# Kernel tuning notes

Measured on AMD Instinct MI355X. Metric: run time of the kernel, lower is better.

Reference implementation:

```python
import jax, jax.numpy as jnp
import numpy as np

B, T, E, H, HD, FF = 2, 2048, 1024, 16, 64, 4096
LN_EPS = 1e-5


def _ln(x, g, b):
    mu = jnp.mean(x, axis=-1, keepdims=True)
    var = jnp.var(x, axis=-1, keepdims=True)
    return (x - mu) * jax.lax.rsqrt(var + LN_EPS) * g + b


def setup_inputs() -> dict:
    key = jax.random.key(0)
    ks = jax.random.split(key, 8)
    s = 0.02
    return {
        "x": jax.random.normal(ks[0], (B, T, E), jnp.float32),
        "Wq": jax.random.normal(ks[1], (H, E, HD), jnp.float32) * s,
        "Wk": jax.random.normal(ks[2], (H, E, HD), jnp.float32) * s,
        "Wv": jax.random.normal(ks[3], (H, E, HD), jnp.float32) * s,
        "Wproj": jax.random.normal(ks[4], (E, E), jnp.float32) * s,
        "bproj": jnp.zeros((E,), jnp.float32),
        "W1": jax.random.normal(ks[5], (E, FF), jnp.float32) * s,
        "b1": jnp.zeros((FF,), jnp.float32),
        "W2": jax.random.normal(ks[6], (FF, E), jnp.float32) * s,
        "b2": jnp.zeros((E,), jnp.float32),
        "g1": jnp.ones((E,), jnp.float32),
        "be1": jnp.zeros((E,), jnp.float32),
        "g2": jnp.ones((E,), jnp.float32),
        "be2": jnp.zeros((E,), jnp.float32),
    }


def reference(x, Wq, Wk, Wv, Wproj, bproj, W1, b1, W2, b2, g1, be1, g2, be2):
    # --- pre-LN multi-head causal self-attention (dropout = eval/identity) ---
    h = _ln(x, g1, be1)  # [B,T,E]
    q = jnp.einsum('btd,hde->bhte', h, Wq)  # [B,H,T,HD]
    k = jnp.einsum('btd,hde->bhte', h, Wk)
    v = jnp.einsum('btd,hde->bhte', h, Wv)
    # NOTE: original code scales by C**-0.5 where C = embedding_dim (not head_size)
    scale = E ** (-0.5)
    wei = jnp.einsum('bhqe,bhke->bhqk', q, k) * scale  # [B,H,T,T]
    causal = jnp.tril(jnp.ones((T, T), dtype=bool))
    wei = jnp.where(causal, wei, -jnp.inf)
    attn = jax.nn.softmax(wei, axis=-1)
    o = jnp.einsum('bhqk,bhke->bhqe', attn, v)  # [B,H,T,HD]
    o = o.transpose(0, 2, 1, 3).reshape(B, T, E)  # concat heads
    o = o @ Wproj + bproj
    x = x + o
    # --- ReLU FFN ---
    h2 = _ln(x, g2, be2)
    f = jax.nn.relu(h2 @ W1 + b1) @ W2 + b2
    return x + f
```

## Files before the change

kernel.cpp:

```cpp
#include <hip/hip_runtime.h>
#include <hip/hip_bf16.h>
#include <stdint.h>

#define T_SEQ 2048
#define E_DIM 1024
#define H_NUM 16
#define HD_DIM 64
#define FF_DIM 4096
#define B_NUM 2
#define N_TOK (B_NUM * T_SEQ)

typedef unsigned short ushort_t;
typedef __bf16 bf16x8 __attribute__((ext_vector_type(8)));
typedef float f32x4 __attribute__((ext_vector_type(4)));

__device__ __forceinline__ float bf2f(ushort_t u) {
    return __uint_as_float(((unsigned)u) << 16);
}
__device__ __forceinline__ ushort_t f2bf(float f) {
    unsigned u = __float_as_uint(f);
    u += 0x7fffu + ((u >> 16) & 1u);
    return (ushort_t)(u >> 16);
}
__device__ __forceinline__ float bflo(unsigned u) { return __uint_as_float(u << 16); }
__device__ __forceinline__ float bfhi(unsigned u) { return __uint_as_float(u & 0xffff0000u); }

__device__ __forceinline__ void async_copy16(const ushort_t* g, ushort_t* l) {
    __builtin_amdgcn_global_load_lds(
        (__attribute__((address_space(1))) uint32_t*)(ushort_t*)g,
        (__attribute__((address_space(3))) uint32_t*)l, 16, 0, 0);
}

__global__ __launch_bounds__(256) void ln_kernel(const float* __restrict__ x,
                                                 const float* __restrict__ g,
                                                 const float* __restrict__ be,
                                                 ushort_t* __restrict__ out) {
    __shared__ float red[8];
    const int row = blockIdx.x, tid = threadIdx.x;
    const float* xr = x + (size_t)row * E_DIM;
    float4 v = ((const float4*)xr)[tid];
    float s = v.x + v.y + v.z + v.w;
    float sq = v.x * v.x + v.y * v.y + v.z * v.z + v.w * v.w;
    for (int off = 32; off; off >>= 1) {
        s += __shfl_xor(s, off);
        sq += __shfl_xor(sq, off);
    }
    const int wid = tid >> 6, lane = tid & 63;
    if (lane == 0) { red[wid] = s; red[4 + wid] = sq; }
    __syncthreads();
    s = red[0] + red[1] + red[2] + red[3];
    sq = red[4] + red[5] + red[6] + red[7];
    const float mean = s * (1.0f / E_DIM);
    const float var = sq * (1.0f / E_DIM) - mean * mean;
    const float rstd = rsqrtf(var + 1e-5f);
    float4 gv = ((const float4*)g)[tid];
    float4 bv = ((const float4*)be)[tid];
    unsigned o0 = f2bf((v.x - mean) * rstd * gv.x + bv.x);
    unsigned o1 = f2bf((v.y - mean) * rstd * gv.y + bv.y);
    unsigned o2 = f2bf((v.z - mean) * rstd * gv.z + bv.z);
    unsigned o3 = f2bf((v.w - mean) * rstd * gv.w + bv.w);
    uint2 w;
    w.x = o0 | (o1 << 16);
    w.y = o2 | (o3 << 16);
    ((uint2*)(out + (size_t)row * E_DIM))[tid] = w;
}

__global__ __launch_bounds__(256) void reduce_ln_kernel(const ushort_t* __restrict__ p0,
                                                        const ushort_t* __restrict__ p1,
                                                        const float* __restrict__ x,
                                                        const float* __restrict__ bias,
                                                        const float* __restrict__ g,
                                                        const float* __restrict__ be,
                                                        float* __restrict__ x1,
                                                        ushort_t* __restrict__ h2) {
    __shared__ float red[8];
    const int row = blockIdx.x, tid = threadIdx.x;
    uint2 u0 = ((const uint2*)(p0 + (size_t)row * E_DIM))[tid];
    uint2 u1 = ((const uint2*)(p1 + (size_t)row * E_DIM))[tid];
    float4 xv = ((const float4*)(x + (size_t)row * E_DIM))[tid];
    float4 bv = ((const float4*)bias)[tid];
    float4 v;
    v.x = xv.x + bv.x + bflo(u0.x) + bflo(u1.x);
    v.y = xv.y + bv.y + bfhi(u0.x) + bfhi(u1.x);
    v.z = xv.z + bv.z + bflo(u0.y) + bflo(u1.y);
    v.w = xv.w + bv.w + bfhi(u0.y) + bfhi(u1.y);
    ((float4*)(x1 + (size_t)row * E_DIM))[tid] = v;
    float s = v.x + v.y + v.z + v.w;
    float sq = v.x * v.x + v.y * v.y + v.z * v.z + v.w * v.w;
    for (int off = 32; off; off >>= 1) {
        s += __shfl_xor(s, off);
        sq += __shfl_xor(sq, off);
    }
    const int wid = tid >> 6, lane = tid & 63;
    if (lane == 0) { red[wid] = s; red[4 + wid] = sq; }
    __syncthreads();
    s = red[0] + red[1] + red[2] + red[3];
    sq = red[4] + red[5] + red[6] + red[7];
    const float mean = s * (1.0f / E_DIM);
    const float var = sq * (1.0f / E_DIM) - mean * mean;
    const float rstd = rsqrtf(var + 1e-5f);
    float4 gv = ((const float4*)g)[tid];
    float4 ev = ((const float4*)be)[tid];
    unsigned o0 = f2bf((v.x - mean) * rstd * gv.x + ev.x);
    unsigned o1 = f2bf((v.y - mean) * rstd * gv.y + ev.y);
    unsigned o2 = f2bf((v.z - mean) * rstd * gv.z + ev.z);
    unsigned o3 = f2bf((v.w - mean) * rstd * gv.w + ev.w);
    uint2 w;
    w.x = o0 | (o1 << 16);
    w.y = o2 | (o3 << 16);
    ((uint2*)(h2 + (size_t)row * E_DIM))[tid] = w;
}

__global__ __launch_bounds__(256) void reduce_out_kernel(const ushort_t* __restrict__ p0,
                                                         const ushort_t* __restrict__ p1,
                                                         const float* __restrict__ x1,
                                                         const float* __restrict__ bias,
                                                         float* __restrict__ out) {
    const int row = blockIdx.x, tid = threadIdx.x;
    uint2 u0 = ((const uint2*)(p0 + (size_t)row * E_DIM))[tid];
    uint2 u1 = ((const uint2*)(p1 + (size_t)row * E_DIM))[tid];
    float4 xv = ((const float4*)(x1 + (size_t)row * E_DIM))[tid];
    float4 bv = ((const float4*)bias)[tid];
    float4 v;
    v.x = xv.x + bv.x + bflo(u0.x) + bflo(u1.x);
    v.y = xv.y + bv.y + bfhi(u0.x) + bfhi(u1.x);
    v.z = xv.z + bv.z + bflo(u0.y) + bflo(u1.y);
    v.w = xv.w + bv.w + bfhi(u0.y) + bfhi(u1.y);
    ((float4*)(out + (size_t)row * E_DIM))[tid] = v;
}

__global__ __launch_bounds__(256) void transpose_kernel(const float* __restrict__ in,
                                                        ushort_t* __restrict__ out,
                                                        int R, int C) {
    __shared__ ushort_t tile[32][33];
    const int c0 = blockIdx.x * 32, r0 = blockIdx.y * 32;
    const int tx = threadIdx.x, ty = threadIdx.y;
#pragma unroll
    for (int i = 0; i < 32; i += 8) tile[ty + i][tx] = f2bf(in[(size_t)(r0 + ty + i) * C + (c0 + tx)]);
    __syncthreads();
#pragma unroll
    for (int i = 0; i < 32; i += 8) out[(size_t)(c0 + ty + i) * R + (r0 + tx)] = tile[tx][ty + i];
}

__global__ __launch_bounds__(256) void transpose_qkv_kernel(const float* __restrict__ Wq,
                                                            const float* __restrict__ Wk,
                                                            const float* __restrict__ Wv,
                                                            ushort_t* __restrict__ outT) {
    __shared__ ushort_t tile[32][33];
    const int z = blockIdx.z, m = z >> 4, hh = z & 15;
    const float* in = ((m == 0) ? Wq : ((m == 1) ? Wk : Wv)) + (size_t)hh * E_DIM * HD_DIM;
    ushort_t* out = outT + (size_t)(m * E_DIM + hh * HD_DIM) * E_DIM;
    const int c0 = blockIdx.x * 32, r0 = blockIdx.y * 32;
    const int tx = threadIdx.x, ty = threadIdx.y;
#pragma unroll
    for (int i = 0; i < 32; i += 8) tile[ty + i][tx] = f2bf(in[(size_t)(r0 + ty + i) * HD_DIM + (c0 + tx)]);
    __syncthreads();
#pragma unroll
    for (int i = 0; i < 32; i += 8) out[(size_t)(c0 + ty + i) * E_DIM + (r0 + tx)] = tile[tx][ty + i];
}

template <int MODE, int BK>
__global__ __launch_bounds__(256) void gemm_bt(const ushort_t* __restrict__ A,
                                               const ushort_t* __restrict__ BT,
                                               const float* __restrict__ bias,
                                               const float* __restrict__ resid,
                                               void* __restrict__ C0,
                                               ushort_t* __restrict__ C1,
                                               ushort_t* __restrict__ C2,
                                               int M, int N, int K, int lda) {
    __shared__ __align__(16) ushort_t lds_a[2][128 * BK];
    __shared__ __align__(16) ushort_t lds_b[2][128 * BK];
    const int tid = threadIdx.x;
    const int id = blockIdx.y * gridDim.x + blockIdx.x;
    const int band = id & 7, within = id >> 3;
    const int rpb = gridDim.y >> 3;
    const int by = band * rpb + (within % rpb);
    const int bx = within / rpb;
    const int m0 = by * 128, n0 = bx * 128;
    const int koff = blockIdx.z * K;
    const int wave = tid >> 6, lane = tid & 63;
    const int wm = (wave >> 1) * 64, wn = (wave & 1) * 64;
    const int quad = lane >> 4, l16 = lane & 15;
    f32x4 acc[4][4] = {};

    const int nk = K / BK;
    auto stage = [&](int kt, int buf) {
        const int k0 = koff + kt * BK;
#pragma unroll
        for (int it = 0; it < BK / 16; ++it) {
            const int ci = it * 256 + tid;
            const int kk = ci >> 9;
            const int rem = ci & 511;
            const int r = rem >> 2, kc = rem & 3;
            const int gk = k0 + kk * 32 + kc * 8;
            async_copy16(A + (size_t)(m0 + r) * lda + gk, &lds_a[buf][ci * 8]);
            async_copy16(BT + (size_t)(n0 + r) * lda + gk, &lds_b[buf][ci * 8]);
        }
    };
    stage(0, 0);

#pragma unroll 1
    for (int kt = 0; kt < nk; ++kt) {
        __syncthreads();
        if (kt + 1 < nk) stage(kt + 1, (kt + 1) & 1);
        const ushort_t* la = lds_a[kt & 1];
        const ushort_t* lb = lds_b[kt & 1];
#pragma unroll
        for (int kk = 0; kk < BK / 32; ++kk) {
            const ushort_t* lak = la + kk * 4096;
            const ushort_t* lbk = lb + kk * 4096;
            bf16x8 af[4], bfr[4];
#pragma unroll
            for (int i = 0; i < 4; i++) af[i] = *(const bf16x8*)&lak[(wm + i * 16 + l16) * 32 + quad * 8];
#pragma unroll
            for (int i = 0; i < 4; i++) bfr[i] = *(const bf16x8*)&lbk[(wn + i * 16 + l16) * 32 + quad * 8];
#pragma unroll
            for (int im = 0; im < 4; im++)
#pragma unroll
                for (int in = 0; in < 4; in++)
                    acc[im][in] = __builtin_amdgcn_mfma_f32_16x16x32_bf16(af[im], bfr[in], acc[im][in], 0, 0, 0);
        }
    }

    ushort_t* pc = nullptr;
    if (MODE == 3) pc = (blockIdx.z == 0) ? (ushort_t*)C0 : C1;
#pragma unroll
    for (int im = 0; im < 4; im++) {
#pragma unroll
        for (int in = 0; in < 4; in++) {
            const int col = n0 + wn + in * 16 + l16;
            float bv = (MODE == 1 || MODE == 2) ? bias[col] : 0.0f;
#pragma unroll
            for (int r = 0; r < 4; r++) {
                const int row = m0 + wm + im * 16 + quad * 4 + r;
                float v = acc[im][in][r] + bv;
                if (MODE == 2) v = fmaxf(v, 0.0f);
                if (MODE == 1) v += resid[(size_t)row * N + col];
                if (MODE == 0) {
                    const int mat = col >> 10, c = col & 1023, hh = c >> 6, d = c & 63;
                    const int bb = row >> 11, tt = row & 2047;
                    const int bh = bb * H_NUM + hh;
                    size_t idx;
                    ushort_t* dst;
                    if (mat == 0) {
                        idx = ((((size_t)bh * 32 + (tt >> 6)) * 8 + (d >> 3)) * 64 + (tt & 63)) * 8 + (d & 7);
                        dst = (ushort_t*)C0;
                        v *= 0.0450842048f;
                    } else if (mat == 1) {
                        idx = ((((size_t)bh * 32 + (tt >> 6)) * 8 + (d >> 3)) * 64 + (tt & 63)) * 8 + (d & 7);
                        dst = C1;
                    } else {
                        idx = ((((size_t)bh * 32 + (tt >> 6)) * 8 + ((tt & 63) >> 3)) * 64 + d) * 8 + (tt & 7);
                        dst = C2;
                    }
                    dst[idx] = f2bf(v);
                } else if (MODE == 1) {
                    ((float*)C0)[(size_t)row * N + col] = v;
                } else if (MODE == 2) {
                    ((ushort_t*)C0)[(size_t)row * N + col] = f2bf(v);
                } else {
                    pc[(size_t)row * N + col] = f2bf(v);
                }
            }
        }
    }
    (void)M;
}

__global__ __launch_bounds__(256, 2) void attn_flash(const ushort_t* __restrict__ qP,
                                                     const ushort_t* __restrict__ kP,
                                                     const ushort_t* __restrict__ vP,
                                                     ushort_t* __restrict__ o) {
    __shared__ __align__(16) ushort_t P_lds[4][32 * 72];
    __shared__ __align__(16) float Ored[2][32][68];
    __shared__ float Lred[2][32];
    const int h = blockIdx.x, p = blockIdx.y, b = blockIdx.z;
    const int bh = b * H_NUM + h;
    const int tid = threadIdx.x;
    const int wave = tid >> 6, lane = tid & 63;
    const int wr = wave >> 1, ws = wave & 1;
    const int quad = lane >> 4, l16 = lane & 15;
    ushort_t* Pw = P_lds[wave];
    const ushort_t* kbase = kP + (size_t)bh * 32 * 4096;
    const ushort_t* vbase = vP + (size_t)bh * 32 * 4096;
    bf16x8 onesf;
#pragma unroll
    for (int j = 0; j < 8; ++j) onesf[j] = (__bf16)1.0f;

#pragma unroll 1
    for (int phase = 0; phase < 2; ++phase) {
        const int qt = (phase == 0) ? (31 - p) : p;
        const int nkt = qt + 1;
        const ushort_t* qbase = qP + ((size_t)bh * 32 + qt) * 4096;
        bf16x8 qf[2][2];
#pragma unroll
        for (int rg = 0; rg < 2; ++rg)
#pragma unroll
            for (int kk = 0; kk < 2; ++kk)
                qf[rg][kk] = *(const bf16x8*)&qbase[((kk * 4 + quad) * 64 + wr * 32 + rg * 16 + l16) * 8];
        f32x4 oacc[2][4] = {};
        f32x4 lacc[2] = {};
        __syncthreads();
        bf16x8 kf[8], vf[8];
        {
            const ushort_t* kb = kbase + (size_t)ws * 4096;
#pragma unroll
            for (int i = 0; i < 8; ++i)
                kf[i] = *(const bf16x8*)&kb[(((i >> 2) * 4 + quad) * 64 + (i & 3) * 16 + l16) * 8];
        }
#pragma unroll 1
        for (int kt = ws; kt < nkt; kt += 2) {
            f32x4 sacc[2][4] = {};
            __builtin_amdgcn_s_setprio(1);
#pragma unroll
            for (int kk = 0; kk < 2; ++kk)
#pragma unroll
                for (int kg = 0; kg < 4; ++kg)
#pragma unroll
                    for (int rg = 0; rg < 2; ++rg)
                        sacc[rg][kg] = __builtin_amdgcn_mfma_f32_16x16x32_bf16(
                            qf[rg][kk], kf[kk * 4 + kg], sacc[rg][kg], 0, 0, 0);
            __builtin_amdgcn_s_setprio(0);
            {
                const ushort_t* vb = vbase + (size_t)kt * 4096;
#pragma unroll
                for (int i = 0; i < 8; ++i)
                    vf[i] = *(const bf16x8*)&vb[(((i >> 2) * 4 + quad) * 64 + (i & 3) * 16 + l16) * 8];
            }
            if (kt + 2 < nkt) {
                const ushort_t* kb = kbase + (size_t)(kt + 2) * 4096;
#pragma unroll
                for (int i = 0; i < 8; ++i)
                    kf[i] = *(const bf16x8*)&kb[(((i >> 2) * 4 + quad) * 64 + (i & 3) * 16 + l16) * 8];
            }
#pragma unroll
            for (int rg = 0; rg < 2; ++rg)
#pragma unroll
                for (int kg = 0; kg < 4; ++kg) {
                    f32x4 sv = sacc[rg][kg];
                    if (kt == qt) {
                        const int jc = kg * 16 + l16;
#pragma unroll
                        for (int r = 0; r < 4; ++r)
                            if (jc > wr * 32 + rg * 16 + quad * 4 + r) sv[r] = -3.0e38f;
                    }
#pragma unroll
                    for (int r = 0; r < 4; ++r) {
                        const float e = exp2f(sv[r]);
                        Pw[(rg * 16 + quad * 4 + r) * 72 + kg * 16 + l16] =
                            (ushort_t)(__float_as_uint(e) >> 16);
                    }
                }
            __builtin_amdgcn_s_setprio(1);
#pragma unroll
            for (int kk = 0; kk < 2; ++kk)
#pragma unroll
                for (int rg = 0; rg < 2; ++rg) {
                    bf16x8 pf = *(const bf16x8*)&Pw[(rg * 16 + l16) * 72 + kk * 32 + quad * 8];
                    lacc[rg] = __builtin_amdgcn_mfma_f32_16x16x32_bf16(pf, onesf, lacc[rg], 0, 0, 0);
#pragma unroll
                    for (int dg = 0; dg < 4; ++dg)
                        oacc[rg][dg] = __builtin_amdgcn_mfma_f32_16x16x32_bf16(
                            pf, vf[kk * 4 + dg], oacc[rg][dg], 0, 0, 0);
                }
            __builtin_amdgcn_s_setprio(0);
        }
        if (ws == 1) {
#pragma unroll
            for (int rg = 0; rg < 2; ++rg) {
#pragma unroll
                for (int dg = 0; dg < 4; ++dg)
#pragma unroll
                    for (int r = 0; r < 4; ++r)
                        Ored[wr][rg * 16 + quad * 4 + r][dg * 16 + l16] = oacc[rg][dg][r];
                if (l16 == 0) {
#pragma unroll
                    for (int r = 0; r < 4; ++r)
                        Lred[wr][rg * 16 + quad * 4 + r] = lacc[rg][r];
                }
            }
        }
        __syncthreads();
        if (ws == 0) {
#pragma unroll
            for (int rg = 0; rg < 2; ++rg)
#pragma unroll
                for (int r = 0; r < 4; ++r) {
                    const int rr = rg * 16 + quad * 4 + r;
                    const float inv = 1.0f / (lacc[rg][r] + Lred[wr][rr]);
                    const int trow = qt * 64 + wr * 32 + rr;
#pragma unroll
                    for (int dg = 0; dg < 4; ++dg) {
                        const float v = oacc[rg][dg][r] + Ored[wr][rr][dg * 16 + l16];
                        o[(size_t)(b * T_SEQ + trow) * E_DIM + h * HD_DIM + dg * 16 + l16] =
                            f2bf(v * inv);
                    }
                }
        }
    }
}

extern "C" void kernel_launch(void* const* d_in, const int* in_sizes, int n_in,
                              void* d_out, int out_size, void* d_ws, size_t ws_size,
                              hipStream_t stream) {
    const float* x = (const float*)d_in[0];
    const float* Wq = (const float*)d_in[1];
    const float* Wk = (const float*)d_in[2];
    const float* Wv = (const float*)d_in[3];
    const float* Wproj = (const float*)d_in[4];
    const float* bproj = (const float*)d_in[5];
    const float* W1 = (const float*)d_in[6];
    const float* b1 = (const float*)d_in[7];
    const float* W2 = (const float*)d_in[8];
    const float* b2 = (const float*)d_in[9];
    const float* g1 = (const float*)d_in[10];
    const float* be1 = (const float*)d_in[11];
    const float* g2 = (const float*)d_in[12];
    const float* be2 = (const float*)d_in[13];

    char* ws = (char*)d_ws;
    const size_t MB = 1024 * 1024;
    ushort_t* W2T    = (ushort_t*)(ws + 0 * MB);
    float*    x1     = (float*)   (ws + 8 * MB);
    ushort_t* W1T    = (ushort_t*)(ws + 24 * MB);
    ushort_t* WprojT = (ushort_t*)(ws + 32 * MB);
    ushort_t* hln    = (ushort_t*)(ws + 34 * MB);
    ushort_t* ocat   = hln;
    ushort_t* WqkvT  = (ushort_t*)(ws + 42 * MB);
    ushort_t* qP     = (ushort_t*)(ws + 48 * MB);
    ushort_t* kP     = (ushort_t*)(ws + 56 * MB);
    ushort_t* vP     = (ushort_t*)(ws + 64 * MB);
    ushort_t* h2     = (ushort_t*)(ws + 72 * MB);
    ushort_t* f1     = (ushort_t*)(ws + 34 * MB);
    ushort_t* pp0    = (ushort_t*)(ws + 48 * MB);
    ushort_t* pp1    = (ushort_t*)(ws + 56 * MB);
    ushort_t* fp0    = (ushort_t*)(ws + 66 * MB);
    ushort_t* fp1    = (ushort_t*)(ws + 24 * MB);
    (void)ws_size; (void)in_sizes; (void)n_in; (void)out_size;

    const dim3 tb(32, 8, 1);
    transpose_qkv_kernel<<<dim3(2, 32, 48), tb, 0, stream>>>(Wq, Wk, Wv, WqkvT);
    transpose_kernel<<<dim3(32, 32, 1), tb, 0, stream>>>(Wproj, WprojT, E_DIM, E_DIM);
    transpose_kernel<<<dim3(128, 32, 1), tb, 0, stream>>>(W1, W1T, E_DIM, FF_DIM);
    transpose_kernel<<<dim3(32, 128, 1), tb, 0, stream>>>(W2, W2T, FF_DIM, E_DIM);

    ln_kernel<<<N_TOK, 256, 0, stream>>>(x, g1, be1, hln);
    gemm_bt<0, 32><<<dim3(24, 32), 256, 0, stream>>>(hln, WqkvT, nullptr, nullptr,
                                                     qP, kP, vP, N_TOK, 3 * E_DIM, E_DIM, E_DIM);
    attn_flash<<<dim3(16, 16, 2), 256, 0, stream>>>(qP, kP, vP, ocat);
    gemm_bt<3, 64><<<dim3(8, 32, 2), 256, 0, stream>>>(ocat, WprojT, nullptr, nullptr,
                                                       pp0, pp1, nullptr, N_TOK, E_DIM, 512, E_DIM);
    reduce_ln_kernel<<<N_TOK, 256, 0, stream>>>(pp0, pp1, x, bproj, g2, be2, x1, h2);
    gemm_bt<2, 64><<<dim3(32, 32), 256, 0, stream>>>(h2, W1T, b1, nullptr,
                                                     f1, nullptr, nullptr, N_TOK, FF_DIM, E_DIM, E_DIM);
    gemm_bt<3, 64><<<dim3(8, 32, 2), 256, 0, stream>>>(f1, W2T, nullptr, nullptr,
                                                       fp0, fp1, nullptr, N_TOK, E_DIM, 2048, FF_DIM);
    reduce_out_kernel<<<N_TOK, 256, 0, stream>>>(fp0, fp1, x1, b2, (float*)d_out);
}
```

Before: 325.4 us.

## Add 256x256-tile pipelined GEMM kernel for FFN first layer

Replaces the generic gemm_bt call for the FFN up-projection (h2 @ W1 + bias, ReLU) with a dedicated 512-thread kernel. It uses 256x256 output tiles, XOR-swizzled LDS, double-buffered async copies with B prefetched two steps ahead, MFMA interleaved with staged loads, and a banded block-index remap for L2 locality. The larger tile raises data reuse per block and aims to overlap global loads with matrix math. In exchange it uses 64KB of LDS, a large accumulator register footprint and only 256 blocks, which may limit occupancy and leave compute units underused.

```diff
diff --git a/kernel.cpp b/kernel.cpp
--- a/kernel.cpp
+++ b/kernel.cpp
@@ -267,6 +267,123 @@
     (void)M;
 }
 
+__global__ __launch_bounds__(512, 2) void gemm256_ffn1(const ushort_t* __restrict__ A,
+                                                       const ushort_t* __restrict__ BT,
+                                                       const float* __restrict__ bias,
+                                                       ushort_t* __restrict__ C,
+                                                       int N, int K, int lda) {
+    __shared__ __align__(16) ushort_t lds_a[2][16384];
+    __shared__ __align__(16) ushort_t lds_b[2][16384];
+    const int tid = threadIdx.x;
+    const int id = blockIdx.y * gridDim.x + blockIdx.x;
+    const int band = id & 7, within = id >> 3;
+    const int rpb = gridDim.y >> 3;
+    const int by = band * rpb + (within % rpb);
+    const int bx = within / rpb;
+    const int m0 = by * 256, n0 = bx * 256;
+    const int wave = tid >> 6, lane = tid & 63;
+    const int wr = wave >> 2, wc = wave & 3;
+    const int quad = lane >> 4, l16 = lane & 15;
+    const int nkt = K >> 6;
+
+    f32x4 acc[8][4] = {};
+
+    auto stageA = [&](int kt, int half) {
+        ushort_t* dst = &lds_a[kt & 1][half * 8192];
+        const ushort_t* src = A + (size_t)(m0 + half * 128) * lda + kt * 64;
+#pragma unroll
+        for (int it = 0; it < 2; ++it) {
+            const int ci = it * 512 + tid;
+            const int r = ci >> 3, c = ci & 7;
+            async_copy16(src + (size_t)r * lda + ((c ^ (r & 7)) << 3), dst + ci * 8);
+        }
+    };
+    auto stageB = [&](int kt, int half) {
+        ushort_t* dst = &lds_b[kt & 1][half * 8192];
+        const ushort_t* src = BT + (size_t)(n0 + half * 128) * lda + kt * 64;
+#pragma unroll
+        for (int it = 0; it < 2; ++it) {
+            const int ci = it * 512 + tid;
+            const int r = ci >> 3, c = ci & 7;
+            async_copy16(src + (size_t)r * lda + ((c ^ (r & 7)) << 3), dst + ci * 8);
+        }
+    };
+
+    stageA(0, 0); stageA(0, 1);
+    stageB(0, 0); stageB(0, 1);
+    stageB(1, 0); stageB(1, 1);
+    asm volatile("s_waitcnt vmcnt(4)" ::: "memory");
+    __builtin_amdgcn_s_barrier();
+
+    const int swz = l16 & 7;
+
+#pragma unroll 1
+    for (int kt = 0; kt < nkt; ++kt) {
+        const int buf = kt & 1;
+        const ushort_t* la = &lds_a[buf][wr * 8192];
+        const ushort_t* lb = &lds_b[buf][(wc >> 1) * 8192];
+        const int brow = (wc & 1) * 64;
+        bf16x8 bfrag[2][4];
+#pragma unroll
+        for (int p = 0; p < 4; ++p) {
+            bf16x8 af[2][2];
+#pragma unroll
+            for (int s = 0; s < 2; ++s) {
+                const int r = (p * 2 + s) * 16 + l16;
+#pragma unroll
+                for (int kk = 0; kk < 2; ++kk)
+                    af[s][kk] = *(const bf16x8*)&la[r * 64 + (((kk << 2) + quad) ^ swz) * 8];
+            }
+            if (p == 0) {
+#pragma unroll
+                for (int kk = 0; kk < 2; ++kk)
+#pragma unroll
+                    for (int fn = 0; fn < 4; ++fn) {
+                        const int r = brow + fn * 16 + l16;
+                        bfrag[kk][fn] = *(const bf16x8*)&lb[r * 64 + (((kk << 2) + quad) ^ swz) * 8];
+                    }
+            }
+            if (p == 0) { if (kt + 1 < nkt) stageA(kt + 1, 0); }
+            else if (p == 1) { if (kt + 1 < nkt) stageA(kt + 1, 1); }
+            else if (p == 2) { if (kt + 2 < nkt) stageB(kt + 2, 0); }
+            else { if (kt + 2 < nkt) stageB(kt + 2, 1); }
+
+            __builtin_amdgcn_s_barrier();
+            asm volatile("s_waitcnt lgkmcnt(0)" ::: "memory");
+            __builtin_amdgcn_sched_barrier(0);
+            __builtin_amdgcn_s_setprio(1);
+#pragma unroll
+            for (int s = 0; s < 2; ++s)
+#pragma unroll
+                for (int kk = 0; kk < 2; ++kk)
+#pragma unroll
+                    for (int fn = 0; fn < 4; ++fn)
+                        acc[p * 2 + s][fn] = __builtin_amdgcn_mfma_f32_16x16x32_bf16(
+                            af[s][kk], bfrag[kk][fn], acc[p * 2 + s][fn], 0, 0, 0);
+            __builtin_amdgcn_s_setprio(0);
+            if (p == 3) {
+                if (kt + 2 < nkt) asm volatile("s_waitcnt vmcnt(4)" ::: "memory");
+                else              asm volatile("s_waitcnt vmcnt(0)" ::: "memory");
+            }
+            __builtin_amdgcn_s_barrier();
+        }
+    }
+
+#pragma unroll
+    for (int fn = 0; fn < 4; ++fn) {
+        const int col = n0 + wc * 64 + fn * 16 + l16;
+        const float bv = bias[col];
+#pragma unroll
+        for (int fm = 0; fm < 8; ++fm) {
+#pragma unroll
+            for (int r = 0; r < 4; ++r) {
+                const int row = m0 + wr * 128 + fm * 16 + quad * 4 + r;
+                C[(size_t)row * N + col] = f2bf(fmaxf(acc[fm][fn][r] + bv, 0.0f));
+            }
+        }
+    }
+}
+
 __global__ __launch_bounds__(256, 2) void attn_flash(const ushort_t* __restrict__ qP,
                                                      const ushort_t* __restrict__ kP,
                                                      const ushort_t* __restrict__ vP,
@@ -451,8 +568,7 @@
     gemm_bt<3, 64><<<dim3(8, 32, 2), 256, 0, stream>>>(ocat, WprojT, nullptr, nullptr,
                                                        pp0, pp1, nullptr, N_TOK, E_DIM, 512, E_DIM);
     reduce_ln_kernel<<<N_TOK, 256, 0, stream>>>(pp0, pp1, x, bproj, g2, be2, x1, h2);
-    gemm_bt<2, 64><<<dim3(32, 32), 256, 0, stream>>>(h2, W1T, b1, nullptr,
-                                                     f1, nullptr, nullptr, N_TOK, FF_DIM, E_DIM, E_DIM);
+    gemm256_ffn1<<<dim3(16, 16), 512, 0, stream>>>(h2, W1T, b1, f1, FF_DIM, E_DIM, E_DIM);
     gemm_bt<3, 64><<<dim3(8, 32, 2), 256, 0, stream>>>(f1, W2T, nullptr, nullptr,
                                                        fp0, fp1, nullptr, N_TOK, E_DIM, 2048, FF_DIM);
     reduce_out_kernel<<<N_TOK, 256, 0, stream>>>(fp0, fp1, x1, b2, (float*)d_out);
```

New measurement: 321.7 us. About the same (-1.2%).
